# Kernel optimization log

Measured on AMD Instinct MI355X. Metric: run time of the kernel, lower is better.

## Reference

```python
import jax, jax.numpy as jnp
import numpy as np

NUM_ITERS = 20  # fixed in the original forward: transcribe(dna, iterations=20)


def transcribe(dna_seed, dna_a, dna_b):
    """Fractal DNA decompression: 20 elementwise contractive-map iterations
    over the full weight tensor, starting from the DNA seed."""
    def step(w, ab):
        a, b = ab
        w = a * w + b * jnp.sin(w)
        return w, None
    w, _ = jax.lax.scan(step, dna_seed, (dna_a, dna_b))
    return w  # [out_features, in_features]


def setup_inputs() -> dict:
    key = jax.random.key(0)
    k1, k2, k3, k4, k5 = jax.random.split(key, 5)
    TOKENS, IN_F, OUT_F = 2048, 4096, 4096
    return {
        "x": jax.random.normal(k1, (TOKENS, IN_F), dtype=jnp.float32),
        "dna_seed": jax.random.normal(k2, (OUT_F, IN_F), dtype=jnp.float32),
        "dna_a": jax.random.uniform(k3, (NUM_ITERS,), dtype=jnp.float32),
        "dna_b": jax.random.uniform(k4, (NUM_ITERS,), dtype=jnp.float32),
        "bias": jax.random.normal(k5, (OUT_F,), dtype=jnp.float32),
    }


def reference(x, dna_seed, dna_a, dna_b, bias):
    weight = transcribe(dna_seed, dna_a, dna_b)          # [out, in]
    # F.linear(x, weight, bias) == x @ weight.T + bias
    return jnp.einsum('ti,oi->to', x, weight) + bias     # [tokens, out]
```

## Files before the change

### kernel.cpp

```cpp
#include <hip/hip_runtime.h>

typedef __attribute__((ext_vector_type(8))) short short8;
typedef __attribute__((ext_vector_type(4))) float floatx4;

#define TOKENS 2048
#define IN_F   4096
#define OUT_F  4096
#define NITER  20
#define BK     64

#define INV_2PI 0.15915494309189535f
#define TWO_PI  6.283185307179586f

__device__ __forceinline__ unsigned short f2bf(float f) {
    unsigned int u = __builtin_bit_cast(unsigned int, f);
    u += 0x7fffu + ((u >> 16) & 1u);
    return (unsigned short)(u >> 16);
}

__device__ __forceinline__ void step4(float4& v, float a, float bc) {
    v.x = __builtin_fmaf(bc, __builtin_amdgcn_sinf(v.x), a * v.x);
    v.y = __builtin_fmaf(bc, __builtin_amdgcn_sinf(v.y), a * v.y);
    v.z = __builtin_fmaf(bc, __builtin_amdgcn_sinf(v.z), a * v.z);
    v.w = __builtin_fmaf(bc, __builtin_amdgcn_sinf(v.w), a * v.w);
}

#define WBLOCKS (OUT_F * IN_F / 8 / 256)
#define XBLOCKS (TOKENS * IN_F / 8 / 256)

__global__ __launch_bounds__(256) void transcribe_fused_kernel(
    const float4* __restrict__ seed, const float4* __restrict__ xin,
    const float* __restrict__ da, const float* __restrict__ db,
    short8* __restrict__ w_out, short8* __restrict__ x_out)
{
    const int b = blockIdx.x;
    short8 o;
    if (b < WBLOCKS) {
        int i = b * 256 + threadIdx.x;
        float4 u = seed[2 * i];
        float4 v = seed[2 * i + 1];
        u.x *= INV_2PI; u.y *= INV_2PI; u.z *= INV_2PI; u.w *= INV_2PI;
        v.x *= INV_2PI; v.y *= INV_2PI; v.z *= INV_2PI; v.w *= INV_2PI;
#pragma unroll
        for (int t = 0; t < NITER; t++) {
            float a = da[t], bc = db[t] * INV_2PI;
            step4(u, a, bc);
            step4(v, a, bc);
        }
        o[0] = (short)f2bf(u.x * TWO_PI); o[1] = (short)f2bf(u.y * TWO_PI);
        o[2] = (short)f2bf(u.z * TWO_PI); o[3] = (short)f2bf(u.w * TWO_PI);
        o[4] = (short)f2bf(v.x * TWO_PI); o[5] = (short)f2bf(v.y * TWO_PI);
        o[6] = (short)f2bf(v.z * TWO_PI); o[7] = (short)f2bf(v.w * TWO_PI);
        w_out[i] = o;
    } else {
        int i = (b - WBLOCKS) * 256 + threadIdx.x;
        float4 u = xin[2 * i];
        float4 v = xin[2 * i + 1];
        o[0] = (short)f2bf(u.x); o[1] = (short)f2bf(u.y);
        o[2] = (short)f2bf(u.z); o[3] = (short)f2bf(u.w);
        o[4] = (short)f2bf(v.x); o[5] = (short)f2bf(v.y);
        o[6] = (short)f2bf(v.z); o[7] = (short)f2bf(v.w);
        x_out[i] = o;
    }
}

__device__ __forceinline__ void g2l16(const ushort* g, ushort* l) {
    __builtin_amdgcn_global_load_lds(
        (const __attribute__((address_space(1))) unsigned int*)g,
        (__attribute__((address_space(3))) unsigned int*)l, 16, 0, 0);
}

__global__ __launch_bounds__(256, 2) void gemm_bt_kernel(
    const ushort* __restrict__ A,
    const ushort* __restrict__ B,
    const float* __restrict__ bias,
    float* __restrict__ C)
{
    __shared__ ushort As[2][128 * BK];
    __shared__ ushort Bs[2][128 * BK];

    const int tid  = threadIdx.x;
    const int lane = tid & 63;
    const int wid  = tid >> 6;
    const int bn   = blockIdx.x;
    const int bm   = blockIdx.y;
    const int wm   = (wid >> 1) << 6;
    const int wn   = (wid & 1) << 6;
    const int fm   = lane & 15;
    const int q    = lane >> 4;

    const int gcol = (((lane & 7) ^ (lane >> 3)) << 3);

    const ushort* gA = A + (size_t)(bm * 128) * IN_F;
    const ushort* gB = B + (size_t)(bn * 128) * IN_F;

    floatx4 acc[4][4];
#pragma unroll
    for (int i = 0; i < 4; i++)
#pragma unroll
        for (int j = 0; j < 4; j++)
            acc[i][j] = (floatx4){0.f, 0.f, 0.f, 0.f};

#define STAGE(k0v, bufi)                                                      \
    {                                                                         \
        _Pragma("unroll")                                                     \
        for (int u = 0; u < 4; u++) {                                         \
            const int cb = ((u << 2) | wid) << 6;             \
            const int r  = (cb >> 3) + (lane >> 3);           \
            g2l16(gA + (size_t)r * IN_F + (k0v) + gcol,                       \
                  &As[bufi][cb * 8 + lane * 8]);                              \
            g2l16(gB + (size_t)r * IN_F + (k0v) + gcol,                       \
                  &Bs[bufi][cb * 8 + lane * 8]);                              \
        }                                                                     \
    }

#define COMPUTE(bufi)                                                         \
    {                                                                         \
        _Pragma("unroll")                                                     \
        for (int s = 0; s < 2; s++) {                                         \
            short8 af[4], bf[4];                                              \
            const int sa = (((q + 4 * s) & 7) ^ (fm & 7)) << 3;               \
            _Pragma("unroll")                                                 \
            for (int i = 0; i < 4; i++) {                                     \
                af[i] = *(const short8*)&As[bufi][(wm + i * 16 + fm) * BK + sa]; \
                bf[i] = *(const short8*)&Bs[bufi][(wn + i * 16 + fm) * BK + sa]; \
            }                                                                 \
            _Pragma("unroll")                                                 \
            for (int i = 0; i < 4; i++)                                       \
                _Pragma("unroll")                                             \
                for (int j = 0; j < 4; j++)                                   \
                    acc[i][j] = __builtin_amdgcn_mfma_f32_16x16x32_bf16(      \
                        af[i], bf[j], acc[i][j], 0, 0, 0);                    \
        }                                                                     \
    }

    STAGE(0, 0);
    __syncthreads();
    STAGE(BK, 1);
    COMPUTE(0);
    __syncthreads();
    for (int k0 = 2 * BK; k0 < IN_F; k0 += 2 * BK) {
        STAGE(k0, 0);
        COMPUTE(1);
        __syncthreads();
        STAGE(k0 + BK, 1);
        COMPUTE(0);
        __syncthreads();
    }
    COMPUTE(1);

#undef STAGE
#undef COMPUTE

    const int cn = lane & 15;
    const int cm = (lane >> 4) << 2;
    float bv[4];
#pragma unroll
    for (int j = 0; j < 4; j++)
        bv[j] = bias[bn * 128 + wn + j * 16 + cn];
#pragma unroll
    for (int i = 0; i < 4; i++) {
#pragma unroll
        for (int r = 0; r < 4; r++) {
            int m = bm * 128 + wm + i * 16 + cm + r;
            float* crow = C + (size_t)m * OUT_F + bn * 128 + wn + cn;
#pragma unroll
            for (int j = 0; j < 4; j++)
                crow[j * 16] = acc[i][j][r] + bv[j];
        }
    }
}

extern "C" void kernel_launch(void* const* d_in, const int* in_sizes, int n_in,
                              void* d_out, int out_size, void* d_ws, size_t ws_size,
                              hipStream_t stream) {
    const float* x    = (const float*)d_in[0];
    const float* seed = (const float*)d_in[1];
    const float* da   = (const float*)d_in[2];
    const float* db   = (const float*)d_in[3];
    const float* bias = (const float*)d_in[4];
    float* out        = (float*)d_out;

    ushort* w_bf = (ushort*)d_ws;
    ushort* x_bf = w_bf + (size_t)OUT_F * IN_F;

    transcribe_fused_kernel<<<WBLOCKS + XBLOCKS, 256, 0, stream>>>(
        (const float4*)seed, (const float4*)x, da, db,
        (short8*)w_bf, (short8*)x_bf);

    dim3 grid(OUT_F / 128, TOKENS / 128);
    gemm_bt_kernel<<<grid, 256, 0, stream>>>(x_bf, w_bf, bias, out);
}
```

Measured before the change: 215.8 us.

## Halve GEMM K-tile to 32 and raise occupancy to four blocks per CU

Cuts the GEMM K-step from 64 to 32, which halves LDS use per block, and raises launch bounds to allow four resident blocks per CU. The global-to-LDS staging and the LDS read swizzle are rebuilt for 32-wide rows: each thread now loads two rows of four 8-element segments with an XOR swizzle. The aim is better latency hiding through more resident waves. In exchange it doubles the number of barriers per K, and the 64 fp32 accumulators may come under register pressure at the tighter launch bound.

```diff
diff --git a/kernel.cpp b/kernel.cpp
--- a/kernel.cpp
+++ b/kernel.cpp
@@ -7,7 +7,7 @@
 #define IN_F   4096
 #define OUT_F  4096
 #define NITER  20
-#define BK     64
+#define BK     32
 
 #define INV_2PI 0.15915494309189535f
 #define TWO_PI  6.283185307179586f
@@ -70,7 +70,7 @@
         (__attribute__((address_space(3))) unsigned int*)l, 16, 0, 0);
 }
 
-__global__ __launch_bounds__(256, 2) void gemm_bt_kernel(
+__global__ __launch_bounds__(256, 4) void gemm_bt_kernel(
     const ushort* __restrict__ A,
     const ushort* __restrict__ B,
     const float* __restrict__ bias,
@@ -87,9 +87,12 @@
     const int wm   = (wid >> 1) << 6;
     const int wn   = (wid & 1) << 6;
     const int fm   = lane & 15;
-    const int q    = lane >> 4;
+    const int fkd  = (((lane >> 4) ^ ((fm >> 1) & 3)) << 3);
 
-    const int gcol = (((lane & 7) ^ (lane >> 3)) << 3);
+    const int row0 = tid >> 2;
+    const int psg  = tid & 3;
+    const int gsg  = (psg ^ ((row0 >> 1) & 3)) << 3;
+    const int lsg  = psg << 3;
 
     const ushort* gA = A + (size_t)(bm * 128) * IN_F;
     const ushort* gB = B + (size_t)(bn * 128) * IN_F;
@@ -101,37 +104,32 @@
         for (int j = 0; j < 4; j++)
             acc[i][j] = (floatx4){0.f, 0.f, 0.f, 0.f};
 
-#define STAGE(k0v, bufi)                                                      \
-    {                                                                         \
-        _Pragma("unroll")                                                     \
-        for (int u = 0; u < 4; u++) {                                         \
-            const int cb = ((u << 2) | wid) << 6;             \
-            const int r  = (cb >> 3) + (lane >> 3);           \
-            g2l16(gA + (size_t)r * IN_F + (k0v) + gcol,                       \
-                  &As[bufi][cb * 8 + lane * 8]);                              \
-            g2l16(gB + (size_t)r * IN_F + (k0v) + gcol,                       \
-                  &Bs[bufi][cb * 8 + lane * 8]);                              \
-        }                                                                     \
+#define STAGE(k0v, bufi)                                                       \
+    {                                                                          \
+        g2l16(gA + (size_t)row0 * IN_F + (k0v) + gsg,                          \
+              &As[bufi][row0 * BK + lsg]);                                     \
+        g2l16(gA + (size_t)(row0 + 64) * IN_F + (k0v) + gsg,                   \
+              &As[bufi][(row0 + 64) * BK + lsg]);                              \
+        g2l16(gB + (size_t)row0 * IN_F + (k0v) + gsg,                          \
+              &Bs[bufi][row0 * BK + lsg]);                                     \
+        g2l16(gB + (size_t)(row0 + 64) * IN_F + (k0v) + gsg,                   \
+              &Bs[bufi][(row0 + 64) * BK + lsg]);                              \
     }
 
-#define COMPUTE(bufi)                                                         \
-    {                                                                         \
-        _Pragma("unroll")                                                     \
-        for (int s = 0; s < 2; s++) {                                         \
-            short8 af[4], bf[4];                                              \
-            const int sa = (((q + 4 * s) & 7) ^ (fm & 7)) << 3;               \
-            _Pragma("unroll")                                                 \
-            for (int i = 0; i < 4; i++) {                                     \
-                af[i] = *(const short8*)&As[bufi][(wm + i * 16 + fm) * BK + sa]; \
-                bf[i] = *(const short8*)&Bs[bufi][(wn + i * 16 + fm) * BK + sa]; \
-            }                                                                 \
-            _Pragma("unroll")                                                 \
-            for (int i = 0; i < 4; i++)                                       \
-                _Pragma("unroll")                                             \
-                for (int j = 0; j < 4; j++)                                   \
-                    acc[i][j] = __builtin_amdgcn_mfma_f32_16x16x32_bf16(      \
-                        af[i], bf[j], acc[i][j], 0, 0, 0);                    \
-        }                                                                     \
+#define COMPUTE(bufi)                                                          \
+    {                                                                          \
+        short8 af[4], bf[4];                                                   \
+        _Pragma("unroll")                                                      \
+        for (int i = 0; i < 4; i++) {                                          \
+            af[i] = *(const short8*)&As[bufi][(wm + i * 16 + fm) * BK + fkd];  \
+            bf[i] = *(const short8*)&Bs[bufi][(wn + i * 16 + fm) * BK + fkd];  \
+        }                                                                      \
+        _Pragma("unroll")                                                      \
+        for (int i = 0; i < 4; i++)                                            \
+            _Pragma("unroll")                                                  \
+            for (int j = 0; j < 4; j++)                                        \
+                acc[i][j] = __builtin_amdgcn_mfma_f32_16x16x32_bf16(           \
+                    af[i], bf[j], acc[i][j], 0, 0, 0);                         \
     }
 
     STAGE(0, 0);
```

Result: slower. 246.9 us (+14.4%).
